# Optimization experiments

Measured on AMD Instinct MI355X. Metric: run time of the kernel, lower is better.

## Reference

```python
import jax, jax.numpy as jnp
import numpy as np

B, N, H, E, OBS, A, AFF, EFF = 2, 50000, 64, 1_000_000, 128, 18, 512, 256


def setup_inputs() -> dict:
    key = jax.random.key(0)
    ks = jax.random.split(key, 20)
    s = 0.05  # small init to keep gates/tanh unsaturated
    return {
        "obs": jax.random.normal(ks[0], (B, OBS), jnp.float32),
        "state": jax.random.normal(ks[1], (B, N, H), jnp.float32) * 0.1,
        "W_in": jax.random.normal(ks[2], (OBS, H), jnp.float32) * s,
        "b_in": jnp.zeros((H,), jnp.float32),
        "W_msg": jax.random.normal(ks[3], (H, H), jnp.float32) * s,
        "W_gate": jax.random.normal(ks[4], (2 * H, H), jnp.float32) * s,
        "b_gate": jnp.zeros((H,), jnp.float32),
        "W_cand": jax.random.normal(ks[5], (2 * H, H), jnp.float32) * s,
        "b_cand": jnp.zeros((H,), jnp.float32),
        "W_dec": jax.random.normal(ks[6], (H, H), jnp.float32) * s,
        "b_dec": jnp.zeros((H,), jnp.float32),
        "W_mean": jax.random.normal(ks[7], (H, A), jnp.float32) * s,
        "b_mean": jnp.zeros((A,), jnp.float32),
        "W_ls": jax.random.normal(ks[8], (H, A), jnp.float32) * s,
        "b_ls": jnp.zeros((A,), jnp.float32),
        "src_index": jax.random.randint(ks[9], (E,), 0, N),
        "dst_index": jax.random.randint(ks[10], (E,), 0, N),
        "afferent_idx": jax.random.randint(ks[11], (AFF,), 0, N),
        "efferent_idx": jax.random.randint(ks[12], (EFF,), 0, N),
    }


def reference(obs, state, W_in, b_in, W_msg, W_gate, b_gate, W_cand, b_cand,
              W_dec, b_dec, W_mean, b_mean, W_ls, b_ls,
              src_index, dst_index, afferent_idx, efferent_idx):
    # inject obs projection into afferent node slots
    projected = obs @ W_in + b_in                                   # [B, H]
    injected = jnp.zeros_like(state).at[:, afferent_idx, :].set(projected[:, None, :])
    # gather-project-scatter message passing over the edge list
    src_msgs = state[:, src_index, :] @ W_msg                       # [B, E, H]
    messages = jnp.zeros_like(state).at[:, dst_index, :].add(src_msgs)
    # GRU-style gated update
    combined = messages + injected
    gate_in = jnp.concatenate([state, combined], axis=-1)           # [B, N, 2H]
    z = jax.nn.sigmoid(gate_in @ W_gate + b_gate)
    cand = jnp.tanh(gate_in @ W_cand + b_cand)
    next_state = (1.0 - z) * state + z * cand
    # mean-pool readout over efferent nodes, then policy heads
    readout = next_state[:, efferent_idx, :].mean(axis=1)           # [B, H]
    decoded = jnp.tanh(readout @ W_dec + b_dec)
    mean = decoded @ W_mean + b_mean
    log_std = jnp.clip(decoded @ W_ls + b_ls, -5.0, 2.0)
    return mean, log_std, next_state
```

## Files before the change

kernel.cpp:

```cpp
#include <hip/hip_runtime.h>
#include <hip/hip_bf16.h>

constexpr int kN   = 50000;
constexpr int kH   = 64;
constexpr int kB   = 2;
constexpr int kE   = 1000000;
constexpr int kObs = 128;
constexpr int kA   = 18;
constexpr int kAff = 512;
constexpr int kEff = 256;
constexpr int kNH  = kN * kH;
constexpr int kOutOff = 2 * kB * kA;
constexpr int kRanges = 8;
constexpr int kNr  = kN / kRanges;
constexpr int kChunks = 64;
constexpr int kEc  = kE / kChunks;
constexpr int kHistB = kRanges * kChunks;
constexpr int kPackPerR = (kNr + 127) / 128;
constexpr int kPackBlocks = kRanges * kPackPerR;
constexpr int kWprepBlocks = 20;
constexpr int kScanB = (kN + 255) / 256;
constexpr int kGatB = kRanges * 1563;
constexpr int kUpdPerR = (kNr + 7) / 8;
constexpr int kUpdB = kRanges * kUpdPerR;

typedef __attribute__((ext_vector_type(8))) short short8_t;
typedef __attribute__((ext_vector_type(4))) float f32x4_t;

__device__ __forceinline__ float ldf(const void* p, int i, int f32) {
  if (f32) return ((const float*)p)[i];
  unsigned short u = ((const unsigned short*)p)[i];
  union { unsigned int x; float f; } v; v.x = ((unsigned int)u) << 16; return v.f;
}
__device__ __forceinline__ void stf(void* p, int i, float val, int f32) {
  if (f32) ((float*)p)[i] = val;
  else ((__hip_bfloat16*)p)[i] = __float2bfloat16(val);
}
__device__ __forceinline__ float lo16(unsigned int w) {
  union { unsigned int i; float f; } v; v.i = w << 16; return v.f;
}
__device__ __forceinline__ float hi16(unsigned int w) {
  union { unsigned int i; float f; } v; v.i = w & 0xffff0000u; return v.f;
}
__device__ __forceinline__ float b2f(unsigned short u) {
  union { unsigned int i; float f; } v; v.i = ((unsigned int)u) << 16; return v.f;
}
__device__ __forceinline__ unsigned int f2b(float f) {
  union { float f; unsigned int u; } v; v.f = f;
  unsigned int r = v.u + 0x7fffu + ((v.u >> 16) & 1u);
  return r >> 16;
}
__device__ __forceinline__ float fsig(float x) {
  return __builtin_amdgcn_rcpf(1.f + __expf(-x));
}
__device__ __forceinline__ float ftanh(float x) {
  return 1.f - 2.f * __builtin_amdgcn_rcpf(__expf(2.f * x) + 1.f);
}
__device__ __forceinline__ int detect64(const unsigned short* wprobe, int t) {
  int hits = 0;
  for (int k = 0; k < 4; ++k) {
    unsigned short u = wprobe[(t * 4 + k) * 2];
    int e = (u >> 7) & 0xFF;
    if ((u & 0x7FFFu) != 0 && e >= 108 && e <= 128) hits++;
  }
  for (int off = 32; off; off >>= 1) hits += __shfl_down(hits, off);
  return (hits < 128) ? 1 : 0;
}

extern "C" __global__ __launch_bounds__(1024) void k_prep(
    const unsigned short* __restrict__ wprobe,
    const void* __restrict__ obs,
    const void* __restrict__ W_in,
    const void* __restrict__ b_in,
    const int* __restrict__ aff_idx,
    const int* __restrict__ dst,
    const void* __restrict__ W_msg,
    const void* __restrict__ W_gate,
    const void* __restrict__ W_cand,
    int* __restrict__ dflag,
    int* __restrict__ flags,
    float* __restrict__ projected,
    int* __restrict__ deg_c,
    unsigned short* __restrict__ wt,
    float* __restrict__ eff_acc) {
  __shared__ int sdeg[kNr];
  int t = threadIdx.x, b = blockIdx.x;
  if (b == 0) {
    __shared__ int sflag;
    if (t < 64) { int f = detect64(wprobe, t); if (t == 0) { sflag = f; dflag[0] = f; } }
    for (int i = t; i < kN; i += 1024) flags[i] = 0;
    eff_acc[t] = 0.f;
    __syncthreads();
    int f32 = sflag;
    if (t < kAff) flags[aff_idx[t]] = 1;
    if (t < kB * kH) {
      int bb = t >> 6, h = t & 63;
      float acc = ldf(b_in, h, f32);
      for (int o = 0; o < kObs; ++o)
        acc += ldf(obs, bb * kObs + o, f32) * ldf(W_in, o * kH + h, f32);
      projected[t] = acc;
    }
  } else if (b <= kHistB) {
    int h = b - 1, r = h & 7, c = h >> 3;
    int r0 = r * kNr;
    for (int i = t; i < kNr; i += 1024) sdeg[i] = 0;
    __syncthreads();
    int end = (c + 1) * kEc;
    for (int e = c * kEc + t; e < end; e += 1024) {
      unsigned rel = (unsigned)(dst[e] - r0);
      if (rel < (unsigned)kNr) atomicAdd(&sdeg[rel], 1);
    }
    __syncthreads();
    for (int i = t; i < kNr; i += 1024) deg_c[c * kN + r0 + i] = sdeg[i];
  } else {
    __shared__ int sflag;
    if (t < 64) { int f = detect64(wprobe, t); if (t == 0) sflag = f; }
    __syncthreads();
    int f32 = sflag;
    int i = (b - 1 - kHistB) * 1024 + t;
    if (i < 4096) {
      int n = i >> 6, k = i & 63;
      wt[i] = (unsigned short)f2b(ldf(W_msg, k * 64 + n, f32));
    } else if (i < 12288) {
      int j = i - 4096; int n = j >> 7, k = j & 127;
      wt[i] = (unsigned short)f2b(ldf(W_gate, k * 64 + n, f32));
    } else if (i < 20480) {
      int j = i - 12288; int n = j >> 7, k = j & 127;
      wt[i] = (unsigned short)f2b(ldf(W_cand, k * 64 + n, f32));
    }
  }
}

extern "C" __global__ void k_scan1(const int* __restrict__ deg_c,
                                   int* __restrict__ row_off,
                                   int* __restrict__ partials) {
  __shared__ int sd[256];
  int t = threadIdx.x;
  int n = blockIdx.x * 256 + t;
  int s = 0;
  if (n < kN) {
    for (int c = 0; c < kChunks; ++c) s += deg_c[c * kN + n];
  }
  sd[t] = s;
  __syncthreads();
  for (int off = 1; off < 256; off <<= 1) {
    int v = (t >= off) ? sd[t - off] : 0;
    __syncthreads();
    sd[t] += v;
    __syncthreads();
  }
  int excl = sd[t] - s;
  if (t == 255) partials[blockIdx.x] = sd[255];
  if (n < kN) row_off[n] = excl;
}

extern "C" __global__ void k_scan3(int* __restrict__ row_off,
                                   const int* __restrict__ partials,
                                   int* __restrict__ deg_c) {
  __shared__ int sd[256];
  int t = threadIdx.x;
  int s = 0;
  for (int j = t; j < (int)blockIdx.x; j += 256) s += partials[j];
  sd[t] = s;
  __syncthreads();
  for (int off = 128; off; off >>= 1) {
    if (t < off) sd[t] += sd[t + off];
    __syncthreads();
  }
  int base = sd[0];
  int n = blockIdx.x * 256 + t;
  if (n < kN) {
    int v = row_off[n] + base;
    row_off[n] = v;
    int run = v;
#pragma unroll 8
    for (int c = 0; c < kChunks; ++c) {
      int d = deg_c[c * kN + n];
      deg_c[c * kN + n] = run;
      run += d;
    }
  }
  if (blockIdx.x == 0 && t == 0) row_off[kN] = kE;
}

extern "C" __global__ __launch_bounds__(1024) void k_scatter(
    const int* __restrict__ src,
    const int* __restrict__ dst,
    const int* __restrict__ chunk_base,
    int* __restrict__ sorted_src,
    const unsigned short* __restrict__ wprobe,
    const void* __restrict__ state,
    unsigned int* __restrict__ pack) {
  __shared__ int scur[kNr];
  int t = threadIdx.x;
  if (blockIdx.x < kHistB) {
    int r = blockIdx.x & 7, c = blockIdx.x >> 3;
    int r0 = r * kNr;
    for (int i = t; i < kNr; i += 1024) scur[i] = chunk_base[c * kN + r0 + i];
    __syncthreads();
    int end = (c + 1) * kEc;
    for (int e = c * kEc + t; e < end; e += 1024) {
      unsigned rel = (unsigned)(dst[e] - r0);
      if (rel < (unsigned)kNr) {
        int pos = atomicAdd(&scur[rel], 1);
        sorted_src[pos] = src[e];
      }
    }
  } else {
    __shared__ int sflag;
    if (t < 64) { int f = detect64(wprobe, t); if (t == 0) sflag = f; }
    __syncthreads();
    int f32 = sflag;
    int p = blockIdx.x - kHistB;
    int x = p & 7, j = p >> 3;
    int nb = x * kNr + j * 128;
    int nl = min(nb + 128, (x + 1) * kNr);
    int i = nb * 64 + t * 8;
    if (i < nl * 64) {
      uint4 o0, o1;
      if (!f32) {
        uint4 a = *(const uint4*)((const unsigned short*)state + i);
        uint4 c4 = *(const uint4*)((const unsigned short*)state + kNH + i);
        o0.x = (a.x & 0xffffu) | (c4.x << 16);
        o0.y = (a.x >> 16)     | (c4.x & 0xffff0000u);
        o0.z = (a.y & 0xffffu) | (c4.y << 16);
        o0.w = (a.y >> 16)     | (c4.y & 0xffff0000u);
        o1.x = (a.z & 0xffffu) | (c4.z << 16);
        o1.y = (a.z >> 16)     | (c4.z & 0xffff0000u);
        o1.z = (a.w & 0xffffu) | (c4.w << 16);
        o1.w = (a.w >> 16)     | (c4.w & 0xffff0000u);
      } else {
        const float* sf = (const float*)state;
        unsigned int w[8];
#pragma unroll
        for (int k = 0; k < 8; ++k)
          w[k] = f2b(sf[i + k]) | (f2b(sf[kNH + i + k]) << 16);
        o0 = make_uint4(w[0], w[1], w[2], w[3]);
        o1 = make_uint4(w[4], w[5], w[6], w[7]);
      }
      *(uint4*)&pack[i] = o0;
      *(uint4*)&pack[i + 4] = o1;
    }
  }
}

extern "C" __global__ __launch_bounds__(256) void k_gather(
    const unsigned int* __restrict__ pack,
    const int* __restrict__ row_off,
    const int* __restrict__ sorted_src,
    unsigned int* __restrict__ agg) {
  int wave = threadIdx.x >> 6, lane = threadIdx.x & 63;
  int x = blockIdx.x & 7, j = blockIdx.x >> 3;
  int local = j * 4 + wave;
  if (local >= kNr) return;
  int n = x * kNr + local;
  int s  = row_off[n];
  int en = row_off[n + 1];
  int g = lane >> 4, col = lane & 15;
  const uint4* pk4 = (const uint4*)pack;
  float a0x = 0.f, a0y = 0.f, a0z = 0.f, a0w = 0.f;
  float a1x = 0.f, a1y = 0.f, a1z = 0.f, a1w = 0.f;
  for (int e = s; e < en; e += 8) {
#pragma unroll
    for (int h = 0; h < 2; ++h) {
      int ee = e + h * 4 + g;
      int idx = sorted_src[min(ee, en - 1)];
      uint4 wv = pk4[idx * 16 + col];
      if (ee >= en) { wv.x = 0u; wv.y = 0u; wv.z = 0u; wv.w = 0u; }
      a0x += lo16(wv.x); a1x += hi16(wv.x);
      a0y += lo16(wv.y); a1y += hi16(wv.y);
      a0z += lo16(wv.z); a1z += hi16(wv.z);
      a0w += lo16(wv.w); a1w += hi16(wv.w);
    }
  }
  a0x += __shfl_xor(a0x, 16); a0x += __shfl_xor(a0x, 32);
  a0y += __shfl_xor(a0y, 16); a0y += __shfl_xor(a0y, 32);
  a0z += __shfl_xor(a0z, 16); a0z += __shfl_xor(a0z, 32);
  a0w += __shfl_xor(a0w, 16); a0w += __shfl_xor(a0w, 32);
  a1x += __shfl_xor(a1x, 16); a1x += __shfl_xor(a1x, 32);
  a1y += __shfl_xor(a1y, 16); a1y += __shfl_xor(a1y, 32);
  a1z += __shfl_xor(a1z, 16); a1z += __shfl_xor(a1z, 32);
  a1w += __shfl_xor(a1w, 16); a1w += __shfl_xor(a1w, 32);
  if (g == 0) {
    uint4 o;
    o.x = f2b(a0x) | (f2b(a1x) << 16);
    o.y = f2b(a0y) | (f2b(a1y) << 16);
    o.z = f2b(a0z) | (f2b(a1z) << 16);
    o.w = f2b(a0w) | (f2b(a1w) << 16);
    ((uint4*)agg)[n * 16 + col] = o;
  }
}

extern "C" __global__ __launch_bounds__(64, 6) void k_update(
    const unsigned int* __restrict__ pk,
    const unsigned short* __restrict__ wt,
    const void* __restrict__ b_gate,
    const void* __restrict__ b_cand,
    const unsigned int* __restrict__ agg,
    const int* __restrict__ flags,
    const float* __restrict__ projected,
    const int* __restrict__ dflag,
    void* __restrict__ out,
    const int* __restrict__ eff_idx,
    float* __restrict__ eff_acc) {
  __shared__ uint4 lx4[274];
  __shared__ int smatch[256];
  __shared__ int smcnt;
  unsigned short* lx = (unsigned short*)lx4;
  int f32 = dflag[0];
  int lane = threadIdx.x;
  int q = lane >> 4, l15 = lane & 15;
  int x = blockIdx.x & 7, jb = blockIdx.x >> 3;
  int ndw = x * kNr + jb * 8;
  int rend = (x + 1) * kNr;
  if (ndw >= rend) return;
  if (lane == 0) smcnt = 0;

  const uint4* pk4 = (const uint4*)pk;
  const uint4* ag4 = (const uint4*)agg;
  for (int j = lane; j < 128; j += 64) {
    int ndl = j >> 4, c4 = j & 15;
    int ndg = min(ndw + ndl, rend - 1);
    uint4 pv = pk4[ndg * 16 + c4];
    uint4 av = ag4[ndg * 16 + c4];
    int r0 = 2 * ndl;
    *(uint2*)&lx[r0 * 136 + c4 * 4] =
        make_uint2((pv.x & 0xffffu) | (pv.y << 16), (pv.z & 0xffffu) | (pv.w << 16));
    *(uint2*)&lx[(r0 + 1) * 136 + c4 * 4] =
        make_uint2((pv.x >> 16) | (pv.y & 0xffff0000u), (pv.z >> 16) | (pv.w & 0xffff0000u));
    *(uint2*)&lx[r0 * 136 + 64 + c4 * 4] =
        make_uint2((av.x & 0xffffu) | (av.y << 16), (av.z & 0xffffu) | (av.w << 16));
    *(uint2*)&lx[(r0 + 1) * 136 + 64 + c4 * 4] =
        make_uint2((av.x >> 16) | (av.y & 0xffff0000u), (av.z >> 16) | (av.w & 0xffff0000u));
  }
  __syncthreads();

  const unsigned short* wm = wt;
  const unsigned short* wg = wt + 4096;
  const unsigned short* wc = wt + 12288;

  short8_t a0 = *(const short8_t*)&lx[l15 * 136 + 64 + q * 8];
  short8_t a1 = *(const short8_t*)&lx[l15 * 136 + 96 + q * 8];
  f32x4_t msgc[4];
#pragma unroll
  for (int ct = 0; ct < 4; ++ct) {
    f32x4_t acc = {0.f, 0.f, 0.f, 0.f};
    short8_t b0 = *(const short8_t*)&wm[(ct * 16 + l15) * 64 + q * 8];
    short8_t b1 = *(const short8_t*)&wm[(ct * 16 + l15) * 64 + 32 + q * 8];
    acc = __builtin_amdgcn_mfma_f32_16x16x32_bf16(a0, b0, acc, 0, 0, 0);
    acc = __builtin_amdgcn_mfma_f32_16x16x32_bf16(a1, b1, acc, 0, 0, 0);
    msgc[ct] = acc;
  }
  int nA = ndw + q * 2, nB = nA + 1;
  int flA = (nA < rend) ? flags[nA] : 0;
  int flB = (nB < rend) ? flags[nB] : 0;
#pragma unroll
  for (int ct = 0; ct < 4; ++ct) {
    int col = ct * 16 + l15;
    float pj0 = projected[col], pj1 = projected[64 + col];
#pragma unroll
    for (int r = 0; r < 4; ++r) {
      int row = q * 4 + r;
      int fl = (r < 2) ? flA : flB;
      float inj = fl ? ((row & 1) ? pj1 : pj0) : 0.f;
      lx[row * 136 + 64 + col] = (unsigned short)f2b(msgc[ct][r] + inj);
    }
  }

  short8_t xa[4];
#pragma unroll
  for (int ks = 0; ks < 4; ++ks)
    xa[ks] = *(const short8_t*)&lx[l15 * 136 + ks * 32 + q * 8];
  float ps[16];
#pragma unroll
  for (int ct = 0; ct < 4; ++ct)
#pragma unroll
    for (int rp = 0; rp < 2; ++rp) {
      int row = q * 4 + 2 * rp;
      ps[ct * 4 + rp * 2 + 0] = b2f(lx[row * 136 + ct * 16 + l15]);
      ps[ct * 4 + rp * 2 + 1] = b2f(lx[(row + 1) * 136 + ct * 16 + l15]);
    }
  float* soutw = (float*)lx4;
#pragma unroll
  for (int ct = 0; ct < 4; ++ct) {
    f32x4_t accg = {0.f, 0.f, 0.f, 0.f}, accc = {0.f, 0.f, 0.f, 0.f};
#pragma unroll
    for (int ks = 0; ks < 4; ++ks) {
      short8_t bg = *(const short8_t*)&wg[(ct * 16 + l15) * 128 + ks * 32 + q * 8];
      short8_t bc = *(const short8_t*)&wc[(ct * 16 + l15) * 128 + ks * 32 + q * 8];
      accg = __builtin_amdgcn_mfma_f32_16x16x32_bf16(xa[ks], bg, accg, 0, 0, 0);
      accc = __builtin_amdgcn_mfma_f32_16x16x32_bf16(xa[ks], bc, accc, 0, 0, 0);
    }
    int col = ct * 16 + l15;
    float bgv = ldf(b_gate, col, f32), bcv = ldf(b_cand, col, f32);
#pragma unroll
    for (int rp = 0; rp < 2; ++rp) {
      int r = q * 4 + 2 * rp;
      float z0 = fsig(accg[2 * rp] + bgv);
      float c0 = ftanh(accc[2 * rp] + bcv);
      soutw[r * 64 + col] = (1.f - z0) * ps[ct * 4 + rp * 2 + 0] + z0 * c0;
      float z1 = fsig(accg[2 * rp + 1] + bgv);
      float c1 = ftanh(accc[2 * rp + 1] + bcv);
      soutw[(r + 1) * 64 + col] = (1.f - z1) * ps[ct * 4 + rp * 2 + 1] + z1 * c1;
    }
  }
  __syncthreads();

  int nlim = min(8, rend - ndw);
  for (int i = lane; i < kEff; i += 64) {
    unsigned rel = (unsigned)(eff_idx[i] - ndw);
    if (rel < (unsigned)nlim) { int s = atomicAdd(&smcnt, 1); smatch[s] = (int)rel; }
  }
  __syncthreads();

  int nvalid = nlim * 64;
  if (f32) {
    float* po = (float*)out + kOutOff;
#pragma unroll
    for (int p = 0; p < 2; ++p)
      for (int j = lane * 4; j < nvalid; j += 256) {
        int ndl = j >> 6, c = j & 63;
        float4 v = *(float4*)((char*)lx4 + ((ndl * 2 + p) * 64 + c) * 4);
        *(float4*)(po + p * kNH + ndw * 64 + j) = v;
      }
  } else {
    unsigned short* po = (unsigned short*)out + kOutOff;
#pragma unroll
    for (int p = 0; p < 2; ++p)
      for (int j = lane * 8; j < nvalid; j += 512) {
        int ndl = j >> 6, c = j & 63;
        const char* base = (const char*)lx4 + ((ndl * 2 + p) * 64 + c) * 4;
        float4 v0 = *(const float4*)base;
        float4 v1 = *(const float4*)(base + 16);
        uint4 o;
        o.x = f2b(v0.x) | (f2b(v0.y) << 16);
        o.y = f2b(v0.z) | (f2b(v0.w) << 16);
        o.z = f2b(v1.x) | (f2b(v1.y) << 16);
        o.w = f2b(v1.z) | (f2b(v1.w) << 16);
        *(uint4*)(po + p * kNH + ndw * 64 + j) = o;
      }
  }

  int cnt = smcnt;
  if (cnt) {
    float a0s = 0.f, a1s = 0.f;
    const float* sf = (const float*)lx4;
    for (int m = 0; m < cnt; ++m) {
      int rel = smatch[m];
      float v0 = sf[(rel * 2 + 0) * 64 + lane];
      float v1 = sf[(rel * 2 + 1) * 64 + lane];
      if (!f32) { v0 = b2f((unsigned short)f2b(v0)); v1 = b2f((unsigned short)f2b(v1)); }
      a0s += v0; a1s += v1;
    }
    atomicAdd(&eff_acc[x * 128 + lane], a0s);
    atomicAdd(&eff_acc[x * 128 + 64 + lane], a1s);
  }
}

extern "C" __global__ void k_readout(const void* __restrict__ W_dec,
                                     const void* __restrict__ b_dec,
                                     const void* __restrict__ W_mean,
                                     const void* __restrict__ b_mean,
                                     const void* __restrict__ W_ls,
                                     const void* __restrict__ b_ls,
                                     const float* __restrict__ eff_acc,
                                     const int* __restrict__ dflag,
                                     void* __restrict__ out) {
  __shared__ float ro[128], dec[128];
  int f32 = dflag[0];
  int t = threadIdx.x;
  if (t < 128) {
    float s = 0.f;
#pragma unroll
    for (int r = 0; r < kRanges; ++r) s += eff_acc[r * 128 + t];
    ro[t] = s * (1.f / kEff);
  }
  __syncthreads();
  if (t < 128) {
    int bb = t >> 6, h = t & 63;
    float d = ldf(b_dec, h, f32);
    for (int k = 0; k < 64; ++k) d += ro[bb * 64 + k] * ldf(W_dec, k * 64 + h, f32);
    dec[t] = tanhf(d);
  }
  __syncthreads();
  if (t < kB * kA) {
    int bb = t / kA, a = t % kA;
    float m = ldf(b_mean, a, f32), l = ldf(b_ls, a, f32);
    for (int k = 0; k < 64; ++k) {
      float dv = dec[bb * 64 + k];
      m += dv * ldf(W_mean, k * kA + a, f32);
      l += dv * ldf(W_ls, k * kA + a, f32);
    }
    l = fminf(fmaxf(l, -5.f), 2.f);
    stf(out, t, m, f32);
    stf(out, kB * kA + t, l, f32);
  }
}

extern "C" void kernel_launch(void* const* d_in, const int* in_sizes, int n_in,
                              void* d_out, int out_size, void* d_ws, size_t ws_size,
                              hipStream_t stream) {
  (void)in_sizes; (void)n_in; (void)out_size; (void)ws_size;
  const void* obs    = d_in[0];
  const void* state  = d_in[1];
  const void* W_in   = d_in[2];
  const void* b_in   = d_in[3];
  const void* W_msg  = d_in[4];
  const void* W_gate = d_in[5];
  const void* b_gate = d_in[6];
  const void* W_cand = d_in[7];
  const void* b_cand = d_in[8];
  const void* W_dec  = d_in[9];
  const void* b_dec  = d_in[10];
  const void* W_mean = d_in[11];
  const void* b_mean = d_in[12];
  const void* W_ls   = d_in[13];
  const void* b_ls   = d_in[14];
  const int* src = (const int*)d_in[15];
  const int* dst = (const int*)d_in[16];
  const int* aff = (const int*)d_in[17];
  const int* eff = (const int*)d_in[18];

  int* wsp        = (int*)d_ws;
  int* flags      = wsp;
  int* deg_c      = flags + kN;
  int* row_off    = deg_c + kChunks * kN;
  int* partials   = row_off + (kN + 64);
  int* dflag      = partials + 512;
  float* projected = (float*)(dflag + 16);
  float* eff_acc   = projected + 128;
  int* sorted_src  = (int*)(eff_acc + 1024);
  unsigned int* pk  = (unsigned int*)(sorted_src + kE);
  unsigned int* agg = pk + kNH;
  unsigned short* wt = (unsigned short*)(agg + kNH);

  k_prep<<<1 + kHistB + kWprepBlocks, 1024, 0, stream>>>(
      (const unsigned short*)W_cand, obs, W_in, b_in, aff, dst,
      W_msg, W_gate, W_cand, dflag, flags, projected, deg_c, wt, eff_acc);
  k_scan1<<<kScanB, 256, 0, stream>>>(deg_c, row_off, partials);
  k_scan3<<<kScanB, 256, 0, stream>>>(row_off, partials, deg_c);
  k_scatter<<<kHistB + kPackBlocks, 1024, 0, stream>>>(
      src, dst, deg_c, sorted_src, (const unsigned short*)W_cand, state, pk);
  k_gather<<<kGatB, 256, 0, stream>>>(pk, row_off, sorted_src, agg);
  k_update<<<kUpdB, 64, 0, stream>>>(pk, wt, b_gate, b_cand,
                                     agg, flags, projected, dflag, d_out,
                                     eff, eff_acc);
  k_readout<<<1, 128, 0, stream>>>(W_dec, b_dec, W_mean, b_mean, W_ls, b_ls,
                                   eff_acc, dflag, d_out);
}
```

Baseline: 271.1 us.

## Fuse gather aggregation into GRU update kernel via shared memory

Merges the edge-gather kernel and the update kernel into one 256-thread block that handles 8 nodes. Each of the four waves gathers two nodes' neighbor sums straight into LDS, and then wave 0 runs the MFMA gated update. This removes the agg buffer round trip through global memory and one kernel launch. In exchange, three of the four waves sit idle during the update phase, and the update work per block is serialized behind the gather.

```diff
diff --git a/kernel.cpp b/kernel.cpp
--- a/kernel.cpp
+++ b/kernel.cpp
@@ -20,9 +20,8 @@
 constexpr int kPackBlocks = kRanges * kPackPerR;
 constexpr int kWprepBlocks = 20;
 constexpr int kScanB = (kN + 255) / 256;
-constexpr int kGatB = kRanges * 1563;
-constexpr int kUpdPerR = (kNr + 7) / 8;
-constexpr int kUpdB = kRanges * kUpdPerR;
+constexpr int kGuPerR = (kNr + 7) / 8;
+constexpr int kGuB = kRanges * kGuPerR;
 
 typedef __attribute__((ext_vector_type(8))) short short8_t;
 typedef __attribute__((ext_vector_type(4))) float f32x4_t;
@@ -244,59 +243,13 @@
   }
 }
 
-extern "C" __global__ __launch_bounds__(256) void k_gather(
+extern "C" __global__ __launch_bounds__(256) void k_gupd(
     const unsigned int* __restrict__ pack,
     const int* __restrict__ row_off,
     const int* __restrict__ sorted_src,
-    unsigned int* __restrict__ agg) {
-  int wave = threadIdx.x >> 6, lane = threadIdx.x & 63;
-  int x = blockIdx.x & 7, j = blockIdx.x >> 3;
-  int local = j * 4 + wave;
-  if (local >= kNr) return;
-  int n = x * kNr + local;
-  int s  = row_off[n];
-  int en = row_off[n + 1];
-  int g = lane >> 4, col = lane & 15;
-  const uint4* pk4 = (const uint4*)pack;
-  float a0x = 0.f, a0y = 0.f, a0z = 0.f, a0w = 0.f;
-  float a1x = 0.f, a1y = 0.f, a1z = 0.f, a1w = 0.f;
-  for (int e = s; e < en; e += 8) {
-#pragma unroll
-    for (int h = 0; h < 2; ++h) {
-      int ee = e + h * 4 + g;
-      int idx = sorted_src[min(ee, en - 1)];
-      uint4 wv = pk4[idx * 16 + col];
-      if (ee >= en) { wv.x = 0u; wv.y = 0u; wv.z = 0u; wv.w = 0u; }
-      a0x += lo16(wv.x); a1x += hi16(wv.x);
-      a0y += lo16(wv.y); a1y += hi16(wv.y);
-      a0z += lo16(wv.z); a1z += hi16(wv.z);
-      a0w += lo16(wv.w); a1w += hi16(wv.w);
-    }
-  }
-  a0x += __shfl_xor(a0x, 16); a0x += __shfl_xor(a0x, 32);
-  a0y += __shfl_xor(a0y, 16); a0y += __shfl_xor(a0y, 32);
-  a0z += __shfl_xor(a0z, 16); a0z += __shfl_xor(a0z, 32);
-  a0w += __shfl_xor(a0w, 16); a0w += __shfl_xor(a0w, 32);
-  a1x += __shfl_xor(a1x, 16); a1x += __shfl_xor(a1x, 32);
-  a1y += __shfl_xor(a1y, 16); a1y += __shfl_xor(a1y, 32);
-  a1z += __shfl_xor(a1z, 16); a1z += __shfl_xor(a1z, 32);
-  a1w += __shfl_xor(a1w, 16); a1w += __shfl_xor(a1w, 32);
-  if (g == 0) {
-    uint4 o;
-    o.x = f2b(a0x) | (f2b(a1x) << 16);
-    o.y = f2b(a0y) | (f2b(a1y) << 16);
-    o.z = f2b(a0z) | (f2b(a1z) << 16);
-    o.w = f2b(a0w) | (f2b(a1w) << 16);
-    ((uint4*)agg)[n * 16 + col] = o;
-  }
-}
-
-extern "C" __global__ __launch_bounds__(64, 6) void k_update(
-    const unsigned int* __restrict__ pk,
     const unsigned short* __restrict__ wt,
     const void* __restrict__ b_gate,
     const void* __restrict__ b_cand,
-    const unsigned int* __restrict__ agg,
     const int* __restrict__ flags,
     const float* __restrict__ projected,
     const int* __restrict__ dflag,
@@ -307,34 +260,69 @@
   __shared__ int smatch[256];
   __shared__ int smcnt;
   unsigned short* lx = (unsigned short*)lx4;
-  int f32 = dflag[0];
-  int lane = threadIdx.x;
-  int q = lane >> 4, l15 = lane & 15;
+  int t = threadIdx.x;
+  int w = t >> 6, lane = t & 63;
+  int g = lane >> 4, col = lane & 15;
   int x = blockIdx.x & 7, jb = blockIdx.x >> 3;
-  int ndw = x * kNr + jb * 8;
+  int nd0 = x * kNr + jb * 8;
   int rend = (x + 1) * kNr;
-  if (ndw >= rend) return;
-  if (lane == 0) smcnt = 0;
-
-  const uint4* pk4 = (const uint4*)pk;
-  const uint4* ag4 = (const uint4*)agg;
-  for (int j = lane; j < 128; j += 64) {
-    int ndl = j >> 4, c4 = j & 15;
-    int ndg = min(ndw + ndl, rend - 1);
+  if (nd0 >= rend) return;
+  if (t == 0) smcnt = 0;
+
+  const uint4* pk4 = (const uint4*)pack;
+
+  if (lane < 32) {
+    int ndl = 2 * w + (lane >> 4), c4 = lane & 15;
+    int ndg = min(nd0 + ndl, rend - 1);
     uint4 pv = pk4[ndg * 16 + c4];
-    uint4 av = ag4[ndg * 16 + c4];
     int r0 = 2 * ndl;
     *(uint2*)&lx[r0 * 136 + c4 * 4] =
         make_uint2((pv.x & 0xffffu) | (pv.y << 16), (pv.z & 0xffffu) | (pv.w << 16));
     *(uint2*)&lx[(r0 + 1) * 136 + c4 * 4] =
         make_uint2((pv.x >> 16) | (pv.y & 0xffff0000u), (pv.z >> 16) | (pv.w & 0xffff0000u));
-    *(uint2*)&lx[r0 * 136 + 64 + c4 * 4] =
-        make_uint2((av.x & 0xffffu) | (av.y << 16), (av.z & 0xffffu) | (av.w << 16));
-    *(uint2*)&lx[(r0 + 1) * 136 + 64 + c4 * 4] =
-        make_uint2((av.x >> 16) | (av.y & 0xffff0000u), (av.z >> 16) | (av.w & 0xffff0000u));
+  }
+#pragma unroll
+  for (int sub = 0; sub < 2; ++sub) {
+    int ndl = 2 * w + sub;
+    int n = nd0 + ndl;
+    if (n >= rend) break;
+    int s = row_off[n], en = row_off[n + 1];
+    float a0x = 0.f, a0y = 0.f, a0z = 0.f, a0w = 0.f;
+    float a1x = 0.f, a1y = 0.f, a1z = 0.f, a1w = 0.f;
+    for (int e = s; e < en; e += 8) {
+#pragma unroll
+      for (int h = 0; h < 2; ++h) {
+        int ee = e + h * 4 + g;
+        int idx = sorted_src[min(ee, en - 1)];
+        uint4 wv = pk4[idx * 16 + col];
+        if (ee >= en) { wv.x = 0u; wv.y = 0u; wv.z = 0u; wv.w = 0u; }
+        a0x += lo16(wv.x); a1x += hi16(wv.x);
+        a0y += lo16(wv.y); a1y += hi16(wv.y);
+        a0z += lo16(wv.z); a1z += hi16(wv.z);
+        a0w += lo16(wv.w); a1w += hi16(wv.w);
+      }
+    }
+    a0x += __shfl_xor(a0x, 16); a0x += __shfl_xor(a0x, 32);
+    a0y += __shfl_xor(a0y, 16); a0y += __shfl_xor(a0y, 32);
+    a0z += __shfl_xor(a0z, 16); a0z += __shfl_xor(a0z, 32);
+    a0w += __shfl_xor(a0w, 16); a0w += __shfl_xor(a0w, 32);
+    a1x += __shfl_xor(a1x, 16); a1x += __shfl_xor(a1x, 32);
+    a1y += __shfl_xor(a1y, 16); a1y += __shfl_xor(a1y, 32);
+    a1z += __shfl_xor(a1z, 16); a1z += __shfl_xor(a1z, 32);
+    a1w += __shfl_xor(a1w, 16); a1w += __shfl_xor(a1w, 32);
+    if (g == 0) {
+      int r0 = 2 * ndl;
+      *(uint2*)&lx[r0 * 136 + 64 + col * 4] =
+          make_uint2(f2b(a0x) | (f2b(a0y) << 16), f2b(a0z) | (f2b(a0w) << 16));
+      *(uint2*)&lx[(r0 + 1) * 136 + 64 + col * 4] =
+          make_uint2(f2b(a1x) | (f2b(a1y) << 16), f2b(a1z) | (f2b(a1w) << 16));
+    }
   }
   __syncthreads();
-
+  if (w != 0) return;
+
+  int f32 = dflag[0];
+  int q = g, l15 = col;
   const unsigned short* wm = wt;
   const unsigned short* wg = wt + 4096;
   const unsigned short* wc = wt + 12288;
@@ -351,19 +339,19 @@
     acc = __builtin_amdgcn_mfma_f32_16x16x32_bf16(a1, b1, acc, 0, 0, 0);
     msgc[ct] = acc;
   }
-  int nA = ndw + q * 2, nB = nA + 1;
+  int nA = nd0 + q * 2, nB = nA + 1;
   int flA = (nA < rend) ? flags[nA] : 0;
   int flB = (nB < rend) ? flags[nB] : 0;
 #pragma unroll
   for (int ct = 0; ct < 4; ++ct) {
-    int col = ct * 16 + l15;
-    float pj0 = projected[col], pj1 = projected[64 + col];
+    int c2 = ct * 16 + l15;
+    float pj0 = projected[c2], pj1 = projected[64 + c2];
 #pragma unroll
     for (int r = 0; r < 4; ++r) {
       int row = q * 4 + r;
       int fl = (r < 2) ? flA : flB;
       float inj = fl ? ((row & 1) ? pj1 : pj0) : 0.f;
-      lx[row * 136 + 64 + col] = (unsigned short)f2b(msgc[ct][r] + inj);
+      lx[row * 136 + 64 + c2] = (unsigned short)f2b(msgc[ct][r] + inj);
     }
   }
 
@@ -391,27 +379,25 @@
       accg = __builtin_amdgcn_mfma_f32_16x16x32_bf16(xa[ks], bg, accg, 0, 0, 0);
       accc = __builtin_amdgcn_mfma_f32_16x16x32_bf16(xa[ks], bc, accc, 0, 0, 0);
     }
-    int col = ct * 16 + l15;
-    float bgv = ldf(b_gate, col, f32), bcv = ldf(b_cand, col, f32);
+    int c2 = ct * 16 + l15;
+    float bgv = ldf(b_gate, c2, f32), bcv = ldf(b_cand, c2, f32);
 #pragma unroll
     for (int rp = 0; rp < 2; ++rp) {
       int r = q * 4 + 2 * rp;
       float z0 = fsig(accg[2 * rp] + bgv);
       float c0 = ftanh(accc[2 * rp] + bcv);
-      soutw[r * 64 + col] = (1.f - z0) * ps[ct * 4 + rp * 2 + 0] + z0 * c0;
+      soutw[r * 64 + c2] = (1.f - z0) * ps[ct * 4 + rp * 2 + 0] + z0 * c0;
       float z1 = fsig(accg[2 * rp + 1] + bgv);
       float c1 = ftanh(accc[2 * rp + 1] + bcv);
-      soutw[(r + 1) * 64 + col] = (1.f - z1) * ps[ct * 4 + rp * 2 + 1] + z1 * c1;
-    }
-  }
-  __syncthreads();
-
-  int nlim = min(8, rend - ndw);
+      soutw[(r + 1) * 64 + c2] = (1.f - z1) * ps[ct * 4 + rp * 2 + 1] + z1 * c1;
+    }
+  }
+
+  int nlim = min(8, rend - nd0);
   for (int i = lane; i < kEff; i += 64) {
-    unsigned rel = (unsigned)(eff_idx[i] - ndw);
+    unsigned rel = (unsigned)(eff_idx[i] - nd0);
     if (rel < (unsigned)nlim) { int s = atomicAdd(&smcnt, 1); smatch[s] = (int)rel; }
   }
-  __syncthreads();
 
   int nvalid = nlim * 64;
   if (f32) {
@@ -421,7 +407,7 @@
       for (int j = lane * 4; j < nvalid; j += 256) {
         int ndl = j >> 6, c = j & 63;
         float4 v = *(float4*)((char*)lx4 + ((ndl * 2 + p) * 64 + c) * 4);
-        *(float4*)(po + p * kNH + ndw * 64 + j) = v;
+        *(float4*)(po + p * kNH + nd0 * 64 + j) = v;
       }
   } else {
     unsigned short* po = (unsigned short*)out + kOutOff;
@@ -437,7 +423,7 @@
         o.y = f2b(v0.z) | (f2b(v0.w) << 16);
         o.z = f2b(v1.x) | (f2b(v1.y) << 16);
         o.w = f2b(v1.z) | (f2b(v1.w) << 16);
-        *(uint4*)(po + p * kNH + ndw * 64 + j) = o;
+        *(uint4*)(po + p * kNH + nd0 * 64 + j) = o;
       }
   }
 
@@ -531,8 +517,7 @@
   float* eff_acc   = projected + 128;
   int* sorted_src  = (int*)(eff_acc + 1024);
   unsigned int* pk  = (unsigned int*)(sorted_src + kE);
-  unsigned int* agg = pk + kNH;
-  unsigned short* wt = (unsigned short*)(agg + kNH);
+  unsigned short* wt = (unsigned short*)(pk + kNH);
 
   k_prep<<<1 + kHistB + kWprepBlocks, 1024, 0, stream>>>(
       (const unsigned short*)W_cand, obs, W_in, b_in, aff, dst,
@@ -541,10 +526,8 @@
   k_scan3<<<kScanB, 256, 0, stream>>>(row_off, partials, deg_c);
   k_scatter<<<kHistB + kPackBlocks, 1024, 0, stream>>>(
       src, dst, deg_c, sorted_src, (const unsigned short*)W_cand, state, pk);
-  k_gather<<<kGatB, 256, 0, stream>>>(pk, row_off, sorted_src, agg);
-  k_update<<<kUpdB, 64, 0, stream>>>(pk, wt, b_gate, b_cand,
-                                     agg, flags, projected, dflag, d_out,
-                                     eff, eff_acc);
+  k_gupd<<<kGuB, 256, 0, stream>>>(pk, row_off, sorted_src, wt, b_gate, b_cand,
+                                   flags, projected, dflag, d_out, eff, eff_acc);
   k_readout<<<1, 128, 0, stream>>>(W_dec, b_dec, W_mean, b_mean, W_ls, b_ls,
                                    eff_acc, dflag, d_out);
 }
```

After: 253.7 us. -6.4%, faster.
